# Kernel optimization log

Hardware: AMD Instinct MI355X
Metric: run time of the kernel (lower is better)

## Reference

```python
import jax, jax.numpy as jnp
import numpy as np

NEG_SLOPE = 0.2


def _gat(x, W, a_src, a_dst, bias, src, dst, nonself, N):
    # PyG GATConv (eval mode): h = x @ W -> [N,H,C]; per-edge scores with
    # LeakyReLU, softmax over incoming edges per target node (self loops
    # re-added after removing any existing ones), weighted scatter-add.
    H, C = a_src.shape
    h = (x @ W).reshape(N, H, C)
    al_s = jnp.einsum('nhc,hc->nh', h, a_src)  # [N,H]
    al_d = jnp.einsum('nhc,hc->nh', h, a_dst)
    e = jax.nn.leaky_relu(al_s[src] + al_d[dst], NEG_SLOPE)  # [E,H]
    e = jnp.where(nonself[:, None], e, -jnp.inf)  # drop input self loops
    e_self = jax.nn.leaky_relu(al_s + al_d, NEG_SLOPE)  # added self loops [N,H]
    m = jnp.maximum(jax.ops.segment_max(e, dst, num_segments=N), e_self)
    w = jnp.exp(e - m[dst])  # masked edges -> 0
    w_self = jnp.exp(e_self - m)
    num = jax.ops.segment_sum(w[:, :, None] * h[src], dst, num_segments=N)
    num = num + w_self[:, :, None] * h
    den = jax.ops.segment_sum(w, dst, num_segments=N) + w_self
    return (num / den[:, :, None]).reshape(N, H * C) + bias


def setup_inputs() -> dict:
    N, E = 100000, 3200000
    key = jax.random.key(0)
    ks = jax.random.split(key, 20)
    s = 0.1
    return {
        'x1': jax.random.normal(ks[0], (N, 7), jnp.float32),
        'x2': jax.random.normal(ks[1], (N, 1), jnp.float32),
        'edge_index': jax.random.randint(ks[2], (2, E), 0, N, jnp.int64)
            if jax.config.jax_enable_x64 else jax.random.randint(ks[2], (2, E), 0, N, jnp.int32),
        'num_nodes': N,
        'lin1_w': s * jax.random.normal(ks[3], (1, 7), jnp.float32),
        'lin1_b': s * jax.random.normal(ks[4], (1,), jnp.float32),
        'lin2_w': s * jax.random.normal(ks[5], (1, 8), jnp.float32),
        'W1': s * jax.random.normal(ks[6], (1, 32), jnp.float32),
        'a_src1': s * jax.random.normal(ks[7], (8, 4), jnp.float32),
        'a_dst1': s * jax.random.normal(ks[8], (8, 4), jnp.float32),
        'b1': s * jax.random.normal(ks[9], (32,), jnp.float32),
        'W2': s * jax.random.normal(ks[10], (32, 16), jnp.float32),
        'a_src2': s * jax.random.normal(ks[11], (4, 4), jnp.float32),
        'a_dst2': s * jax.random.normal(ks[12], (4, 4), jnp.float32),
        'b2': s * jax.random.normal(ks[13], (16,), jnp.float32),
        'W3': s * jax.random.normal(ks[14], (16, 8), jnp.float32),
        'a_src3': s * jax.random.normal(ks[15], (2, 4), jnp.float32),
        'a_dst3': s * jax.random.normal(ks[16], (2, 4), jnp.float32),
        'b3': s * jax.random.normal(ks[17], (8,), jnp.float32),
    }


def reference(x1, x2, edge_index, num_nodes, lin1_w, lin1_b, lin2_w,
              W1, a_src1, a_dst1, b1, W2, a_src2, a_dst2, b2,
              W3, a_src3, a_dst3, b3):
    N = num_nodes
    src, dst = edge_index[0], edge_index[1]
    nonself = src != dst
    # init score + 3 GAT layers (dropouts inactive in eval mode)
    h0 = jax.nn.relu(x1 @ lin1_w.T + lin1_b)  # [N,1]
    x3 = jax.nn.relu(_gat(h0, W1, a_src1, a_dst1, b1, src, dst, nonself, N))
    x4 = jax.nn.relu(_gat(x3, W2, a_src2, a_dst2, b2, src, dst, nonself, N))
    x6 = jax.nn.relu(_gat(x4, W3, a_src3, a_dst3, b3, src, dst, nonself, N))  # [N,8]
    # Row-normalized adjacency with diagonal filled to 1 (sparse form of the
    # original dense Adj): Adj[i,j] = 1/deg[i] on edges (i!=j) and diagonal.
    ns = nonself.astype(x6.dtype)
    deg = 1.0 + jax.ops.segment_sum(ns, src, num_segments=N)  # [N]
    # local score: rowsum(Adj * (x6 x6^T))
    dots = jnp.sum(x6[src] * x6[dst], axis=-1) * ns  # [E]
    local = (jax.ops.segment_sum(dots, src, num_segments=N)
             + jnp.sum(x6 * x6, axis=-1)) / deg  # [N]
    # global score: lin2(Adj @ x6)
    R3 = (jax.ops.segment_sum(x6[dst] * ns[:, None], src, num_segments=N)
          + x6) / deg[:, None]  # [N,8]
    return local[:, None] + R3 @ lin2_w.T  # [N,1]
```

## Files before the change

kernel.cpp:

```cpp
#include <hip/hip_runtime.h>
#include <hip/hip_fp16.h>
#include <math.h>

static constexpr float NEG_SLOPE = 0.2f;
static constexpr int P      = 256;
static constexpr int MAXNPR = 400;
static constexpr int CAP    = 14000;
static constexpr int CHSZ   = 4096;

__device__ __forceinline__ float lrelu(float x) { return x > 0.0f ? x : NEG_SLOPE * x; }

__device__ __forceinline__ void dm(int x, unsigned int mg, int npr, int& r, int& lk) {
    r = (int)__umulhi((unsigned int)x, mg);
    lk = x - r * npr;
    if (lk >= npr) { lk -= npr; ++r; }
    else if (lk < 0) { lk += npr; --r; }
}

union H8 { int4 i4; __half2 h2[4]; };

__device__ __forceinline__ void h8_to_f(int4 v, float* o) {
    H8 u; u.i4 = v;
#pragma unroll
    for (int k = 0; k < 4; ++k) {
        float2 f = __half22float2(u.h2[k]);
        o[2 * k] = f.x; o[2 * k + 1] = f.y;
    }
}

__device__ __forceinline__ int4 f_to_h8(const float* s) {
    H8 u;
#pragma unroll
    for (int k = 0; k < 4; ++k)
        u.h2[k] = __float22half2_rn(make_float2(s[2 * k], s[2 * k + 1]));
    return u.i4;
}

__global__ __launch_bounds__(256) void part2_kernel(
    const int* __restrict__ src, const int* __restrict__ dst,
    int* __restrict__ gcount,
    unsigned int* __restrict__ stgd, unsigned int* __restrict__ stgs,
    int E, int npr, unsigned int mg)
{
    __shared__ int cnt[2 * P];
    __shared__ int base[2 * P];
    __shared__ int pref[P + 1];
    __shared__ int tick[P];
    __shared__ int scn[P];
    __shared__ unsigned int buf[CHSZ];
    const int c = blockIdx.x;
    const int i0 = c * CHSZ;
    const int i1 = min(i0 + CHSZ, E);
    const int tot = i1 - i0;
    const int tid = threadIdx.x;
    cnt[tid] = 0; cnt[P + tid] = 0;
    __syncthreads();
    const int nv = (tot > 0) ? (tot >> 2) : 0;
    const int4* s4 = (const int4*)(src + i0);
    const int4* d4 = (const int4*)(dst + i0);
    for (int t = tid; t < nv; t += 256) {
        int4 s = s4[t], d = d4[t];
        int r, lk;
        dm(d.x, mg, npr, r, lk); atomicAdd(&cnt[r], 1);
        dm(d.y, mg, npr, r, lk); atomicAdd(&cnt[r], 1);
        dm(d.z, mg, npr, r, lk); atomicAdd(&cnt[r], 1);
        dm(d.w, mg, npr, r, lk); atomicAdd(&cnt[r], 1);
        dm(s.x, mg, npr, r, lk); atomicAdd(&cnt[P + r], 1);
        dm(s.y, mg, npr, r, lk); atomicAdd(&cnt[P + r], 1);
        dm(s.z, mg, npr, r, lk); atomicAdd(&cnt[P + r], 1);
        dm(s.w, mg, npr, r, lk); atomicAdd(&cnt[P + r], 1);
    }
    for (int i = i0 + (nv << 2) + tid; i < i1; i += 256) {
        int s = src[i], d = dst[i];
        int r, lk;
        dm(d, mg, npr, r, lk); atomicAdd(&cnt[r], 1);
        dm(s, mg, npr, r, lk); atomicAdd(&cnt[P + r], 1);
    }
    __syncthreads();
    base[tid]     = atomicAdd(&gcount[tid],     cnt[tid]);
    base[P + tid] = atomicAdd(&gcount[P + tid], cnt[P + tid]);
    __syncthreads();
#pragma unroll
    for (int dir = 0; dir < 2; ++dir) {
        const int* key = dir ? (src + i0) : (dst + i0);
        const int* val = dir ? (dst + i0) : (src + i0);
        unsigned int* stg = dir ? stgs : stgd;
        int v = cnt[dir * P + tid];
        scn[tid] = v;
        __syncthreads();
#pragma unroll
        for (int off = 1; off < P; off <<= 1) {
            int t = (tid >= off) ? scn[tid - off] : 0;
            __syncthreads();
            scn[tid] += t;
            __syncthreads();
        }
        int ex = scn[tid] - v;
        pref[tid] = ex;
        tick[tid] = ex;
        if (tid == 0) pref[P] = tot;
        __syncthreads();
        for (int i = tid; i < tot; i += 256) {
            int r, lk;
            dm(key[i], mg, npr, r, lk);
            int p = atomicAdd(&tick[r], 1);
            buf[p] = ((unsigned int)lk << 17) | (unsigned int)val[i];
        }
        __syncthreads();
        for (int i = tid; i < tot; i += 256) {
            int lo = 0, hi = P;
            while (hi - lo > 1) {
                int mid = (lo + hi) >> 1;
                if (pref[mid] <= i) lo = mid; else hi = mid;
            }
            int b = base[dir * P + lo] + (i - pref[lo]);
            if (b < CAP) stg[(size_t)lo * CAP + b] = buf[i];
        }
        __syncthreads();
    }
}

__global__ __launch_bounds__(512) void ebase_kernel(
    const int* __restrict__ gtot, int* __restrict__ ebase)
{
    __shared__ int sm[2 * P];
    int tid = threadIdx.x;
    int v = gtot[tid];
    sm[tid] = v;
    __syncthreads();
#pragma unroll
    for (int off = 1; off < P; off <<= 1) {
        int t = ((tid & (P - 1)) >= off) ? sm[tid - off] : 0;
        __syncthreads();
        sm[tid] += t;
        __syncthreads();
    }
    ebase[tid] = sm[tid] - v;
}

__global__ __launch_bounds__(256) void build_kernel(
    const unsigned int* __restrict__ stgd, const unsigned int* __restrict__ stgs,
    const int* __restrict__ gtot, const int* __restrict__ ebase,
    int* __restrict__ col_dst, int* __restrict__ col_src,
    int* __restrict__ deg_dst, int* __restrict__ deg_src,
    int* __restrict__ row_dst, int* __restrict__ row_src,
    int N, int npr)
{
    __shared__ int cnt[MAXNPR];
    __shared__ int pref[MAXNPR];
    __shared__ int part[256];
    __shared__ int outv[CAP];
    const int dir = blockIdx.x >> 8;
    const int r = blockIdx.x & (P - 1);
    const unsigned int* stg = (dir ? stgs : stgd) + (size_t)r * CAP;
    int tot = gtot[dir * P + r];
    if (tot > CAP) tot = CAP;
    const int n0 = r * npr;
    const int nb = min(npr, N - n0);
    const int tid = threadIdx.x;
    for (int j = tid; j < npr; j += 256) cnt[j] = 0;
    __syncthreads();
    for (int i = tid; i < tot; i += 256)
        atomicAdd(&cnt[stg[i] >> 17], 1);
    __syncthreads();
    int b0 = tid * 4;
    int v0 = 0, v1 = 0, v2 = 0, v3 = 0;
    if (b0 + 0 < npr) v0 = cnt[b0 + 0];
    if (b0 + 1 < npr) v1 = cnt[b0 + 1];
    if (b0 + 2 < npr) v2 = cnt[b0 + 2];
    if (b0 + 3 < npr) v3 = cnt[b0 + 3];
    int s = v0 + v1 + v2 + v3;
    part[tid] = s;
    __syncthreads();
#pragma unroll
    for (int off = 1; off < 256; off <<= 1) {
        int t = (tid >= off) ? part[tid - off] : 0;
        __syncthreads();
        part[tid] += t;
        __syncthreads();
    }
    int ex = part[tid] - s;
    if (b0 + 0 < npr) pref[b0 + 0] = ex;
    if (b0 + 1 < npr) pref[b0 + 1] = ex + v0;
    if (b0 + 2 < npr) pref[b0 + 2] = ex + v0 + v1;
    if (b0 + 3 < npr) pref[b0 + 3] = ex + v0 + v1 + v2;
    __syncthreads();
    int* deg = dir ? deg_src : deg_dst;
    int* row = dir ? row_src : row_dst;
    const int eb = ebase[dir * P + r];
    for (int j = tid; j < nb; j += 256) {
        deg[n0 + j] = cnt[j];
        row[n0 + j] = eb + pref[j];
    }
    __syncthreads();
    for (int j = tid; j < npr; j += 256) cnt[j] = pref[j];
    __syncthreads();
    for (int i = tid; i < tot; i += 256) {
        unsigned int w = stg[i];
        int t = atomicAdd(&cnt[w >> 17], 1);
        outv[t] = (int)(w & 0x1FFFFu);
    }
    __syncthreads();
    int* col = (dir ? col_src : col_dst) + eb;
    for (int i = tid; i < tot; i += 256) col[i] = outv[i];
}

__global__ __launch_bounds__(256) void l1h0_kernel(
    const float* __restrict__ x1, const float* __restrict__ lin1_w,
    const float* __restrict__ lin1_b, float* __restrict__ h0, int N)
{
    int n = blockIdx.x * blockDim.x + threadIdx.x;
    if (n >= N) return;
    float acc = lin1_b[0];
#pragma unroll
    for (int k = 0; k < 7; ++k) acc = fmaf(x1[n * 7 + k], lin1_w[k], acc);
    h0[n] = fmaxf(acc, 0.0f);
}

__global__ __launch_bounds__(256) void gat_gather1_kernel(
    const int* __restrict__ row_start, const int* __restrict__ degv,
    const int* __restrict__ col, const float* __restrict__ h0,
    const float* __restrict__ W1, const float* __restrict__ a_src,
    const float* __restrict__ a_dst, const float* __restrict__ bias,
    float* __restrict__ x3, int N)
{
    int t = blockIdx.x * 256 + threadIdx.x;
    int n = t >> 3, lane = t & 7;
    if (n >= N) return;
    float cs[8], cd[8];
#pragma unroll
    for (int hd = 0; hd < 8; ++hd) {
        float s = 0.0f, d = 0.0f;
#pragma unroll
        for (int c = 0; c < 4; ++c) {
            s = fmaf(W1[hd * 4 + c], a_src[hd * 4 + c], s);
            d = fmaf(W1[hd * 4 + c], a_dst[hd * 4 + c], d);
        }
        cs[hd] = s; cd[hd] = d;
    }
    float h0n = h0[n];
    float wh[8], den[8], adn[8];
#pragma unroll
    for (int hd = 0; hd < 8; ++hd) {
        adn[hd] = h0n * cd[hd];
        if (lane == 0) {
            float w = __expf(lrelu(h0n * cs[hd] + adn[hd]));
            den[hd] = w; wh[hd] = w * h0n;
        } else { den[hd] = 0.0f; wh[hd] = 0.0f; }
    }
    int start = row_start[n];
    int end = start + degv[n];
    for (int e = start + lane; e < end; e += 8) {
        int s = col[e];
        if (s == n) continue;
        float hs = h0[s];
#pragma unroll
        for (int hd = 0; hd < 8; ++hd) {
            float w = __expf(lrelu(hs * cs[hd] + adn[hd]));
            den[hd] += w;
            wh[hd] = fmaf(w, hs, wh[hd]);
        }
    }
#pragma unroll
    for (int m = 1; m < 8; m <<= 1) {
#pragma unroll
        for (int hd = 0; hd < 8; ++hd) {
            den[hd] += __shfl_xor(den[hd], m);
            wh[hd]  += __shfl_xor(wh[hd], m);
        }
    }
    float fct = wh[lane] / den[lane];
    const float4 wv = ((const float4*)W1)[lane];
    const float4 bb = ((const float4*)bias)[lane];
    float4 r;
    r.x = fmaxf(fmaf(fct, wv.x, bb.x), 0.0f);
    r.y = fmaxf(fmaf(fct, wv.y, bb.y), 0.0f);
    r.z = fmaxf(fmaf(fct, wv.z, bb.z), 0.0f);
    r.w = fmaxf(fmaf(fct, wv.w, bb.w), 0.0f);
    ((float4*)x3)[(size_t)n * 8 + lane] = r;
}

template <int IN, int HC>
__global__ __launch_bounds__(256) void gat_node_f16_kernel(
    const float* __restrict__ x, const float* __restrict__ W,
    int4* __restrict__ hp, int N)
{
    int n = blockIdx.x * blockDim.x + threadIdx.x;
    if (n >= N) return;
    float xv[IN];
#pragma unroll
    for (int k = 0; k < IN; ++k) xv[k] = x[n * IN + k];
    float hv[HC];
#pragma unroll
    for (int j = 0; j < HC; ++j) {
        float acc = 0.0f;
#pragma unroll
        for (int k = 0; k < IN; ++k) acc = fmaf(xv[k], W[k * HC + j], acc);
        hv[j] = acc;
    }
#pragma unroll
    for (int q = 0; q < HC / 8; ++q)
        hp[(size_t)n * (HC / 8) + q] = f_to_h8(hv + q * 8);
}

__global__ __launch_bounds__(256) void gat_gather2_kernel(
    const int* __restrict__ row_start, const int* __restrict__ degv,
    const int* __restrict__ col, const int4* __restrict__ hp,
    const float* __restrict__ a_src, const float* __restrict__ a_dst,
    const float* __restrict__ bias, float* __restrict__ xout, int N)
{
    int t = blockIdx.x * 256 + threadIdx.x;
    int n = t >> 3, lane = t & 7;
    if (n >= N) return;
    float As[16], Ad[16];
#pragma unroll
    for (int j = 0; j < 16; ++j) { As[j] = a_src[j]; Ad[j] = a_dst[j]; }
    float hn[16];
    h8_to_f(hp[(size_t)n * 2], hn);
    h8_to_f(hp[(size_t)n * 2 + 1], hn + 8);
    float ald[4];
#pragma unroll
    for (int hd = 0; hd < 4; ++hd) {
        float d = 0.0f;
#pragma unroll
        for (int c = 0; c < 4; ++c) d = fmaf(hn[hd * 4 + c], Ad[hd * 4 + c], d);
        ald[hd] = d;
    }
    float num[16], den[4];
    if (lane == 0) {
#pragma unroll
        for (int hd = 0; hd < 4; ++hd) {
            float a = 0.0f;
#pragma unroll
            for (int c = 0; c < 4; ++c) a = fmaf(hn[hd * 4 + c], As[hd * 4 + c], a);
            float w = __expf(lrelu(a + ald[hd]));
            den[hd] = w;
#pragma unroll
            for (int c = 0; c < 4; ++c) num[hd * 4 + c] = w * hn[hd * 4 + c];
        }
    } else {
#pragma unroll
        for (int j = 0; j < 16; ++j) num[j] = 0.0f;
#pragma unroll
        for (int hd = 0; hd < 4; ++hd) den[hd] = 0.0f;
    }
    int start = row_start[n];
    int end = start + degv[n];
    for (int e = start + lane; e < end; e += 8) {
        int s = col[e];
        if (s == n) continue;
        float hs[16];
        h8_to_f(hp[(size_t)s * 2], hs);
        h8_to_f(hp[(size_t)s * 2 + 1], hs + 8);
#pragma unroll
        for (int hd = 0; hd < 4; ++hd) {
            float a = 0.0f;
#pragma unroll
            for (int c = 0; c < 4; ++c) a = fmaf(hs[hd * 4 + c], As[hd * 4 + c], a);
            float w = __expf(lrelu(a + ald[hd]));
            den[hd] += w;
#pragma unroll
            for (int c = 0; c < 4; ++c) num[hd * 4 + c] = fmaf(w, hs[hd * 4 + c], num[hd * 4 + c]);
        }
    }
#pragma unroll
    for (int m = 1; m < 8; m <<= 1) {
#pragma unroll
        for (int hd = 0; hd < 4; ++hd) den[hd] += __shfl_xor(den[hd], m);
#pragma unroll
        for (int j = 0; j < 16; ++j) num[j] += __shfl_xor(num[j], m);
    }
    if (lane < 4) {
        float inv = 1.0f / den[lane];
        const float4 bb = ((const float4*)bias)[lane];
        float4 r;
        r.x = fmaxf(fmaf(num[lane * 4 + 0], inv, bb.x), 0.0f);
        r.y = fmaxf(fmaf(num[lane * 4 + 1], inv, bb.y), 0.0f);
        r.z = fmaxf(fmaf(num[lane * 4 + 2], inv, bb.z), 0.0f);
        r.w = fmaxf(fmaf(num[lane * 4 + 3], inv, bb.w), 0.0f);
        ((float4*)xout)[(size_t)n * 4 + lane] = r;
    }
}

__global__ __launch_bounds__(256) void gat_gather3_kernel(
    const int* __restrict__ row_start, const int* __restrict__ degv,
    const int* __restrict__ col, const int4* __restrict__ hp,
    const float* __restrict__ a_src, const float* __restrict__ a_dst,
    const float* __restrict__ bias, int4* __restrict__ x6p, int N)
{
    int t = blockIdx.x * 256 + threadIdx.x;
    int n = t >> 2, lane = t & 3;
    if (n >= N) return;
    float As[8], Ad[8];
#pragma unroll
    for (int j = 0; j < 8; ++j) { As[j] = a_src[j]; Ad[j] = a_dst[j]; }
    float hn[8];
    h8_to_f(hp[n], hn);
    float ald[2];
#pragma unroll
    for (int hd = 0; hd < 2; ++hd) {
        float d = 0.0f;
#pragma unroll
        for (int c = 0; c < 4; ++c) d = fmaf(hn[hd * 4 + c], Ad[hd * 4 + c], d);
        ald[hd] = d;
    }
    float num[8], den[2];
    if (lane == 0) {
#pragma unroll
        for (int hd = 0; hd < 2; ++hd) {
            float a = 0.0f;
#pragma unroll
            for (int c = 0; c < 4; ++c) a = fmaf(hn[hd * 4 + c], As[hd * 4 + c], a);
            float w = __expf(lrelu(a + ald[hd]));
            den[hd] = w;
#pragma unroll
            for (int c = 0; c < 4; ++c) num[hd * 4 + c] = w * hn[hd * 4 + c];
        }
    } else {
#pragma unroll
        for (int j = 0; j < 8; ++j) num[j] = 0.0f;
        den[0] = den[1] = 0.0f;
    }
    int start = row_start[n];
    int end = start + degv[n];
    for (int e = start + lane; e < end; e += 4) {
        int s = col[e];
        if (s == n) continue;
        float hs[8];
        h8_to_f(hp[s], hs);
#pragma unroll
        for (int hd = 0; hd < 2; ++hd) {
            float a = 0.0f;
#pragma unroll
            for (int c = 0; c < 4; ++c) a = fmaf(hs[hd * 4 + c], As[hd * 4 + c], a);
            float w = __expf(lrelu(a + ald[hd]));
            den[hd] += w;
#pragma unroll
            for (int c = 0; c < 4; ++c) num[hd * 4 + c] = fmaf(w, hs[hd * 4 + c], num[hd * 4 + c]);
        }
    }
#pragma unroll
    for (int m = 1; m < 4; m <<= 1) {
        den[0] += __shfl_xor(den[0], m);
        den[1] += __shfl_xor(den[1], m);
#pragma unroll
        for (int j = 0; j < 8; ++j) num[j] += __shfl_xor(num[j], m);
    }
    if (lane == 0) {
        float o[8];
        float i0 = 1.0f / den[0], i1 = 1.0f / den[1];
#pragma unroll
        for (int c = 0; c < 4; ++c) {
            o[c]     = fmaxf(fmaf(num[c], i0, bias[c]), 0.0f);
            o[4 + c] = fmaxf(fmaf(num[4 + c], i1, bias[4 + c]), 0.0f);
        }
        x6p[n] = f_to_h8(o);
    }
}

__global__ __launch_bounds__(256) void score_gather_kernel(
    const int* __restrict__ row_start, const int* __restrict__ degv,
    const int* __restrict__ col, const int4* __restrict__ x6p,
    const float* __restrict__ lin2_w, float* __restrict__ out, int N)
{
    int t = blockIdx.x * 256 + threadIdx.x;
    int n = t >> 2, lane = t & 3;
    if (n >= N) return;
    float sx[8];
    h8_to_f(x6p[n], sx);
    float loc, r[8];
    int sc = 0;
    if (lane == 0) {
        loc = 0.0f;
#pragma unroll
        for (int j = 0; j < 8; ++j) { loc = fmaf(sx[j], sx[j], loc); r[j] = sx[j]; }
    } else {
        loc = 0.0f;
#pragma unroll
        for (int j = 0; j < 8; ++j) r[j] = 0.0f;
    }
    int start = row_start[n];
    int dg = degv[n];
    int end = start + dg;
    for (int e = start + lane; e < end; e += 4) {
        int d = col[e];
        if (d == n) { ++sc; continue; }
        float dx[8];
        h8_to_f(x6p[d], dx);
#pragma unroll
        for (int j = 0; j < 8; ++j) { loc = fmaf(sx[j], dx[j], loc); r[j] += dx[j]; }
    }
#pragma unroll
    for (int m = 1; m < 4; m <<= 1) {
        loc += __shfl_xor(loc, m);
        sc  += __shfl_xor(sc, m);
#pragma unroll
        for (int j = 0; j < 8; ++j) r[j] += __shfl_xor(r[j], m);
    }
    if (lane == 0) {
        float invd = 1.0f / (1.0f + (float)(dg - sc));
        float g = 0.0f;
#pragma unroll
        for (int j = 0; j < 8; ++j) g = fmaf(r[j], lin2_w[j], g);
        out[n] = (loc + g) * invd;
    }
}

extern "C" void kernel_launch(void* const* d_in, const int* in_sizes, int n_in,
                              void* d_out, int out_size, void* d_ws, size_t ws_size,
                              hipStream_t stream)
{
    const float* x1     = (const float*)d_in[0];
    const int*   ei     = (const int*)d_in[2];
    const float* lin1_w = (const float*)d_in[4];
    const float* lin1_b = (const float*)d_in[5];
    const float* lin2_w = (const float*)d_in[6];
    const float* W1     = (const float*)d_in[7];
    const float* a_src1 = (const float*)d_in[8];
    const float* a_dst1 = (const float*)d_in[9];
    const float* b1     = (const float*)d_in[10];
    const float* W2     = (const float*)d_in[11];
    const float* a_src2 = (const float*)d_in[12];
    const float* a_dst2 = (const float*)d_in[13];
    const float* b2     = (const float*)d_in[14];
    const float* W3     = (const float*)d_in[15];
    const float* a_src3 = (const float*)d_in[16];
    const float* a_dst3 = (const float*)d_in[17];
    const float* b3     = (const float*)d_in[18];
    float* out = (float*)d_out;

    const int N = in_sizes[0] / 7;
    const int E = in_sizes[2] / 2;
    const int* src = ei;
    const int* dst = ei + E;

    const int npr = (N + P - 1) / P;
    const unsigned int mg = (unsigned int)((0x100000000ULL + npr - 1) / (unsigned long long)npr);
    const int PB = (E + CHSZ - 1) / CHSZ;

    size_t Ns = (size_t)N, Es = (size_t)E;
    int* ideg_dst = (int*)d_ws;
    int* ideg_src = ideg_dst + Ns;
    int* irow_dst = ideg_src + Ns;
    int* irow_src = irow_dst + Ns;
    int* gcount   = irow_src + Ns;
    int* iebase   = gcount + 2 * P;
    int* icol_dst = iebase + 2 * P;
    int* icol_src = icol_dst + Es;
    float* f = (float*)(icol_src + Es);
    unsigned int* stgd = (unsigned int*)f;
    unsigned int* stgs = stgd + (size_t)P * CAP;
    float* h0  = f;
    float* x3  = f + Ns;
    int4*  h2p = (int4*)(f + 33 * Ns);
    float* x4  = f + 41 * Ns;
    int4*  h3p = (int4*)(f + 57 * Ns);
    int4*  x6p = (int4*)(f + 61 * Ns);

    const int TB = 256;
    const int gN = (N + TB - 1) / TB;
    const int g8 = (8 * N + TB - 1) / TB;
    const int g4 = (4 * N + TB - 1) / TB;

    hipMemsetAsync(gcount, 0, 2 * P * sizeof(int), stream);
    part2_kernel<<<PB, 256, 0, stream>>>(src, dst, gcount, stgd, stgs, E, npr, mg);
    ebase_kernel<<<1, 2 * P, 0, stream>>>(gcount, iebase);
    build_kernel<<<2 * P, 256, 0, stream>>>(stgd, stgs, gcount, iebase,
                                            icol_dst, icol_src,
                                            ideg_dst, ideg_src,
                                            irow_dst, irow_src, N, npr);

    l1h0_kernel<<<gN, TB, 0, stream>>>(x1, lin1_w, lin1_b, h0, N);
    gat_gather1_kernel<<<g8, TB, 0, stream>>>(irow_dst, ideg_dst, icol_dst,
                                              h0, W1, a_src1, a_dst1, b1, x3, N);

    gat_node_f16_kernel<32, 16><<<gN, TB, 0, stream>>>(x3, W2, h2p, N);
    gat_gather2_kernel<<<g8, TB, 0, stream>>>(irow_dst, ideg_dst, icol_dst,
                                              h2p, a_src2, a_dst2, b2, x4, N);

    gat_node_f16_kernel<16, 8><<<gN, TB, 0, stream>>>(x4, W3, h3p, N);
    gat_gather3_kernel<<<g4, TB, 0, stream>>>(irow_dst, ideg_dst, icol_dst,
                                              h3p, a_src3, a_dst3, b3, x6p, N);

    score_gather_kernel<<<g4, TB, 0, stream>>>(irow_src, ideg_src, icol_src,
                                               x6p, lin2_w, out, N);
}
```

Measured before the change: 314.1 us.

## Streamline CSR partition and build: fused scans, precomputed scatter addresses, direct column writes

The partition kernel now runs both prefix scans together and computes each edge's global staging address while bucketing into shared memory, replacing the per-element binary search over bucket prefixes. The build kernel uses 512 threads with one thread per node slot, which simplifies its scan, and it writes column indices straight to global memory instead of staging them in a 14000-entry shared array. This cuts shared-memory use and scan synchronisations, but adds a shared address array in the partition kernel. The build kernel's global column writes are now scattered and no longer coalesced.

```diff
diff --git a/kernel.cpp b/kernel.cpp
--- a/kernel.cpp
+++ b/kernel.cpp
@@ -4,7 +4,6 @@
 
 static constexpr float NEG_SLOPE = 0.2f;
 static constexpr int P      = 256;
-static constexpr int MAXNPR = 400;
 static constexpr int CAP    = 14000;
 static constexpr int CHSZ   = 4096;
 
@@ -44,10 +43,11 @@
 {
     __shared__ int cnt[2 * P];
     __shared__ int base[2 * P];
-    __shared__ int pref[P + 1];
+    __shared__ int s0[P];
+    __shared__ int s1[P];
     __shared__ int tick[P];
-    __shared__ int scn[P];
     __shared__ unsigned int buf[CHSZ];
+    __shared__ unsigned int dsta[CHSZ];
     const int c = blockIdx.x;
     const int i0 = c * CHSZ;
     const int i1 = min(i0 + CHSZ, E);
@@ -77,46 +77,53 @@
         dm(s, mg, npr, r, lk); atomicAdd(&cnt[P + r], 1);
     }
     __syncthreads();
-    base[tid]     = atomicAdd(&gcount[tid],     cnt[tid]);
-    base[P + tid] = atomicAdd(&gcount[P + tid], cnt[P + tid]);
-    __syncthreads();
-#pragma unroll
-    for (int dir = 0; dir < 2; ++dir) {
-        const int* key = dir ? (src + i0) : (dst + i0);
-        const int* val = dir ? (dst + i0) : (src + i0);
-        unsigned int* stg = dir ? stgs : stgd;
-        int v = cnt[dir * P + tid];
-        scn[tid] = v;
+    int c0 = cnt[tid], c1 = cnt[P + tid];
+    base[tid]     = atomicAdd(&gcount[tid],     c0);
+    base[P + tid] = atomicAdd(&gcount[P + tid], c1);
+    s0[tid] = c0; s1[tid] = c1;
+    __syncthreads();
+#pragma unroll
+    for (int off = 1; off < P; off <<= 1) {
+        int t0 = (tid >= off) ? s0[tid - off] : 0;
+        int t1 = (tid >= off) ? s1[tid - off] : 0;
         __syncthreads();
-#pragma unroll
-        for (int off = 1; off < P; off <<= 1) {
-            int t = (tid >= off) ? scn[tid - off] : 0;
-            __syncthreads();
-            scn[tid] += t;
-            __syncthreads();
-        }
-        int ex = scn[tid] - v;
-        pref[tid] = ex;
-        tick[tid] = ex;
-        if (tid == 0) pref[P] = tot;
+        s0[tid] += t0; s1[tid] += t1;
         __syncthreads();
-        for (int i = tid; i < tot; i += 256) {
-            int r, lk;
-            dm(key[i], mg, npr, r, lk);
-            int p = atomicAdd(&tick[r], 1);
-            buf[p] = ((unsigned int)lk << 17) | (unsigned int)val[i];
-        }
-        __syncthreads();
-        for (int i = tid; i < tot; i += 256) {
-            int lo = 0, hi = P;
-            while (hi - lo > 1) {
-                int mid = (lo + hi) >> 1;
-                if (pref[mid] <= i) lo = mid; else hi = mid;
-            }
-            int b = base[dir * P + lo] + (i - pref[lo]);
-            if (b < CAP) stg[(size_t)lo * CAP + b] = buf[i];
-        }
-        __syncthreads();
+    }
+    int ex0 = s0[tid] - c0;
+    int ex1 = s1[tid] - c1;
+    s0[tid] = ex0;
+    s1[tid] = ex1;
+    tick[tid] = ex0;
+    __syncthreads();
+    for (int i = tid; i < tot; i += 256) {
+        int r, lk;
+        dm(dst[i0 + i], mg, npr, r, lk);
+        int p = atomicAdd(&tick[r], 1);
+        buf[p] = ((unsigned int)lk << 17) | (unsigned int)src[i0 + i];
+        int b = base[r] + (p - s0[r]);
+        dsta[p] = (b < CAP) ? (unsigned int)r * CAP + b : 0xFFFFFFFFu;
+    }
+    __syncthreads();
+    for (int i = tid; i < tot; i += 256) {
+        unsigned int a = dsta[i];
+        if (a != 0xFFFFFFFFu) stgd[a] = buf[i];
+    }
+    __syncthreads();
+    tick[tid] = ex1;
+    __syncthreads();
+    for (int i = tid; i < tot; i += 256) {
+        int r, lk;
+        dm(src[i0 + i], mg, npr, r, lk);
+        int p = atomicAdd(&tick[r], 1);
+        buf[p] = ((unsigned int)lk << 17) | (unsigned int)dst[i0 + i];
+        int b = base[P + r] + (p - s1[r]);
+        dsta[p] = (b < CAP) ? (unsigned int)r * CAP + b : 0xFFFFFFFFu;
+    }
+    __syncthreads();
+    for (int i = tid; i < tot; i += 256) {
+        unsigned int a = dsta[i];
+        if (a != 0xFFFFFFFFu) stgs[a] = buf[i];
     }
 }
 
@@ -138,7 +145,7 @@
     ebase[tid] = sm[tid] - v;
 }
 
-__global__ __launch_bounds__(256) void build_kernel(
+__global__ __launch_bounds__(512) void build_kernel(
     const unsigned int* __restrict__ stgd, const unsigned int* __restrict__ stgs,
     const int* __restrict__ gtot, const int* __restrict__ ebase,
     int* __restrict__ col_dst, int* __restrict__ col_src,
@@ -146,10 +153,8 @@
     int* __restrict__ row_dst, int* __restrict__ row_src,
     int N, int npr)
 {
-    __shared__ int cnt[MAXNPR];
-    __shared__ int pref[MAXNPR];
-    __shared__ int part[256];
-    __shared__ int outv[CAP];
+    __shared__ int cnt[512];
+    __shared__ int scn[512];
     const int dir = blockIdx.x >> 8;
     const int r = blockIdx.x & (P - 1);
     const unsigned int* stg = (dir ? stgs : stgd) + (size_t)r * CAP;
@@ -158,51 +163,35 @@
     const int n0 = r * npr;
     const int nb = min(npr, N - n0);
     const int tid = threadIdx.x;
-    for (int j = tid; j < npr; j += 256) cnt[j] = 0;
-    __syncthreads();
-    for (int i = tid; i < tot; i += 256)
+    cnt[tid] = 0;
+    __syncthreads();
+    for (int i = tid; i < tot; i += 512)
         atomicAdd(&cnt[stg[i] >> 17], 1);
     __syncthreads();
-    int b0 = tid * 4;
-    int v0 = 0, v1 = 0, v2 = 0, v3 = 0;
-    if (b0 + 0 < npr) v0 = cnt[b0 + 0];
-    if (b0 + 1 < npr) v1 = cnt[b0 + 1];
-    if (b0 + 2 < npr) v2 = cnt[b0 + 2];
-    if (b0 + 3 < npr) v3 = cnt[b0 + 3];
-    int s = v0 + v1 + v2 + v3;
-    part[tid] = s;
-    __syncthreads();
-#pragma unroll
-    for (int off = 1; off < 256; off <<= 1) {
-        int t = (tid >= off) ? part[tid - off] : 0;
+    int v = cnt[tid];
+    scn[tid] = v;
+    __syncthreads();
+#pragma unroll
+    for (int off = 1; off < 512; off <<= 1) {
+        int t = (tid >= off) ? scn[tid - off] : 0;
         __syncthreads();
-        part[tid] += t;
+        scn[tid] += t;
         __syncthreads();
     }
-    int ex = part[tid] - s;
-    if (b0 + 0 < npr) pref[b0 + 0] = ex;
-    if (b0 + 1 < npr) pref[b0 + 1] = ex + v0;
-    if (b0 + 2 < npr) pref[b0 + 2] = ex + v0 + v1;
-    if (b0 + 3 < npr) pref[b0 + 3] = ex + v0 + v1 + v2;
-    __syncthreads();
-    int* deg = dir ? deg_src : deg_dst;
-    int* row = dir ? row_src : row_dst;
+    int ex = scn[tid] - v;
     const int eb = ebase[dir * P + r];
-    for (int j = tid; j < nb; j += 256) {
-        deg[n0 + j] = cnt[j];
-        row[n0 + j] = eb + pref[j];
-    }
-    __syncthreads();
-    for (int j = tid; j < npr; j += 256) cnt[j] = pref[j];
-    __syncthreads();
-    for (int i = tid; i < tot; i += 256) {
+    if (tid < nb) {
+        (dir ? deg_src : deg_dst)[n0 + tid] = v;
+        (dir ? row_src : row_dst)[n0 + tid] = eb + ex;
+    }
+    cnt[tid] = eb + ex;
+    __syncthreads();
+    int* col = dir ? col_src : col_dst;
+    for (int i = tid; i < tot; i += 512) {
         unsigned int w = stg[i];
         int t = atomicAdd(&cnt[w >> 17], 1);
-        outv[t] = (int)(w & 0x1FFFFu);
-    }
-    __syncthreads();
-    int* col = (dir ? col_src : col_dst) + eb;
-    for (int i = tid; i < tot; i += 256) col[i] = outv[i];
+        col[t] = (int)(w & 0x1FFFFu);
+    }
 }
 
 __global__ __launch_bounds__(256) void l1h0_kernel(
@@ -565,7 +554,7 @@
     hipMemsetAsync(gcount, 0, 2 * P * sizeof(int), stream);
     part2_kernel<<<PB, 256, 0, stream>>>(src, dst, gcount, stgd, stgs, E, npr, mg);
     ebase_kernel<<<1, 2 * P, 0, stream>>>(gcount, iebase);
-    build_kernel<<<2 * P, 256, 0, stream>>>(stgd, stgs, gcount, iebase,
+    build_kernel<<<2 * P, 512, 0, stream>>>(stgd, stgs, gcount, iebase,
                                             icol_dst, icol_src,
                                             ideg_dst, ideg_src,
                                             irow_dst, irow_src, N, npr);
```

Measured after the change: 317.4 us. About the same (+1.0%).
